# Kernel tuning notes

Hardware: AMD Instinct MI355X
Metric: run time of the kernel (lower is better)

Reference implementation:

```python
import jax, jax.numpy as jnp
import numpy as np
import math

B, S, D, H = 4, 2048, 1024, 16
DK = D // H

def setup_inputs() -> dict:
    key = jax.random.key(0)
    ks = jax.random.split(key, 8)
    scale = 1.0 / math.sqrt(D)
    q = jax.random.normal(ks[0], (B, S, D), dtype=jnp.float32)
    k = jax.random.normal(ks[1], (B, S, D), dtype=jnp.float32)
    v = jax.random.normal(ks[2], (B, S, D), dtype=jnp.float32)
    Wq = jax.random.normal(ks[3], (D, D), dtype=jnp.float32) * scale
    Wk = jax.random.normal(ks[4], (D, D), dtype=jnp.float32) * scale
    Wv = jax.random.normal(ks[5], (D, D), dtype=jnp.float32) * scale
    Wo = jax.random.normal(ks[6], (D, D), dtype=jnp.float32) * scale
    # causal mask, broadcast over batch and heads (masked_fill where mask == 0)
    mask = jnp.tril(jnp.ones((S, S), dtype=jnp.int32))[None, None, :, :]
    return {"q": q, "k": k, "v": v, "Wq": Wq, "Wk": Wk, "Wv": Wv, "Wo": Wo, "mask": mask}

def reference(q, k, v, Wq, Wk, Wv, Wo, mask):
    # Linear projections (nn.Linear: x @ W^T), split heads -> [B, H, S, DK]
    def split_heads(x, W):
        y = jnp.einsum('bsd,ed->bse', x, W)
        return y.reshape(x.shape[0], x.shape[1], H, DK).transpose(0, 2, 1, 3)
    qh = split_heads(q, Wq)
    kh = split_heads(k, Wk)
    vh = split_heads(v, Wv)
    scores = jnp.einsum('bhqd,bhkd->bhqk', qh, kh) / math.sqrt(DK)  # [B,H,S,S]
    scores = jnp.where(mask == 0, -jnp.inf, scores)
    p = jax.nn.softmax(scores, axis=-1)
    ctx = jnp.einsum('bhqk,bhkd->bhqd', p, vh)
    ctx = ctx.transpose(0, 2, 1, 3).reshape(q.shape[0], q.shape[1], H * DK)
    return jnp.einsum('bsd,ed->bse', ctx, Wo)
```

## Files before the change

kernel.cpp:

```cpp
#include <hip/hip_runtime.h>

#define BB 4
#define SS 2048
#define DD 1024
#define HH 16
#define DKK 64
#define MTOT (BB * SS)
#define QKV_N (MTOT * DD)
#define W_N (DD * DD)

typedef __attribute__((ext_vector_type(8))) short short8;
typedef __attribute__((ext_vector_type(4))) float f32x4;
typedef __attribute__((ext_vector_type(4))) unsigned short u16x4;
typedef unsigned short ushort_t;

#define GP(p) ((__attribute__((address_space(1))) void*)(p))
#define LP(p) ((__attribute__((address_space(3))) void*)(p))

#if __has_builtin(__builtin_amdgcn_exp2f)
#define EXP2(x) __builtin_amdgcn_exp2f(x)
#else
#define EXP2(x) __expf((x) * 0.6931471805599453f)
#endif
#define QSCALE 0.1803368801111204f

__device__ __forceinline__ ushort_t f2bf(float f) {
    union { float f; unsigned u; } c; c.f = f;
    unsigned r = c.u + 0x7fffu + ((c.u >> 16) & 1u);
    return (ushort_t)(r >> 16);
}

__global__ __launch_bounds__(256)
void cvt2(const float* __restrict__ s0, ushort_t* __restrict__ d0, int n0,
          const float* __restrict__ s1, ushort_t* __restrict__ d1, int n1)
{
    int i = (blockIdx.x * 256 + threadIdx.x) * 4;
    const float* s; ushort_t* d; int off;
    if (i < n0) { s = s0; d = d0; off = i; }
    else        { s = s1; d = d1; off = i - n0; if (off >= n1) return; }
    f32x4 x = *(const f32x4*)(s + off);
    u16x4 h;
    h[0] = f2bf(x[0]); h[1] = f2bf(x[1]); h[2] = f2bf(x[2]); h[3] = f2bf(x[3]);
    *(u16x4*)(d + off) = h;
}

template<int MODE>
__global__ __launch_bounds__(256, 2)
void gemm_m97(const ushort_t* __restrict__ A, const ushort_t* __restrict__ W,
              void* __restrict__ out, float scale)
{
    __shared__ ushort_t As[128 * 32];
    __shared__ ushort_t Bs[128 * 32];

    const int tid  = threadIdx.x;
    const int lane = tid & 63;
    const int w    = tid >> 6;
    const int wm   = w >> 1, wn = w & 1;
    const int l15  = lane & 15, l4 = lane >> 4;
    const int m0   = blockIdx.x * 128;
    const int n0   = blockIdx.y * 128;

    f32x4 acc[4][4] = {};

    for (int kk = 0; kk < 1024; kk += 32) {
        #pragma unroll
        for (int i = 0; i < 2; ++i) {
            int c  = i * 256 + w * 64 + lane;
            int r  = c >> 2;
            int cb = (c & 3) ^ (r & 3);
            __builtin_amdgcn_global_load_lds(
                GP(A + (size_t)(m0 + r) * 1024 + kk + cb * 8), LP(As + c * 8), 16, 0, 0);
            __builtin_amdgcn_global_load_lds(
                GP(W + (size_t)(n0 + r) * 1024 + kk + cb * 8), LP(Bs + c * 8), 16, 0, 0);
        }
        __syncthreads();

        short8 af[4], bfr[4];
        #pragma unroll
        for (int mi = 0; mi < 4; ++mi) {
            int row = wm * 64 + mi * 16 + l15;
            af[mi] = *(const short8*)(As + (row * 4 + (l4 ^ (row & 3))) * 8);
        }
        #pragma unroll
        for (int ni = 0; ni < 4; ++ni) {
            int row = wn * 64 + ni * 16 + l15;
            bfr[ni] = *(const short8*)(Bs + (row * 4 + (l4 ^ (row & 3))) * 8);
        }
        #pragma unroll
        for (int mi = 0; mi < 4; ++mi)
            #pragma unroll
            for (int ni = 0; ni < 4; ++ni)
                acc[mi][ni] = __builtin_amdgcn_mfma_f32_16x16x32_bf16(
                    af[mi], bfr[ni], acc[mi][ni], 0, 0, 0);
        __syncthreads();
    }

    #pragma unroll
    for (int mi = 0; mi < 4; ++mi) {
        int rowb = m0 + wm * 64 + mi * 16 + l4 * 4;
        #pragma unroll
        for (int ni = 0; ni < 4; ++ni) {
            int n = n0 + wn * 64 + ni * 16 + l15;
            if constexpr (MODE == 0) {
                int h = n >> 6, dk = n & 63;
                #pragma unroll
                for (int r = 0; r < 4; ++r) {
                    int m = rowb + r, b = m >> 11, s = m & 2047;
                    ((ushort_t*)out)[(((size_t)(b * 16 + h) * 2048 + s) << 6) + dk] =
                        f2bf(acc[mi][ni][r] * scale);
                }
            } else if constexpr (MODE == 1) {
                int h = n >> 6, dk = n & 63;
                int b = rowb >> 11, s0v = rowb & 2047;
                u16x4 hh;
                #pragma unroll
                for (int r = 0; r < 4; ++r) hh[r] = f2bf(acc[mi][ni][r]);
                *(u16x4*)((ushort_t*)out + (((size_t)(b * 16 + h) << 6) + dk) * 2048 + s0v) = hh;
            } else {
                #pragma unroll
                for (int r = 0; r < 4; ++r)
                    ((float*)out)[(size_t)(rowb + r) * 1024 + n] = acc[mi][ni][r];
            }
        }
    }
}

__global__ __launch_bounds__(256, 2)
void attn_fwd5(const ushort_t* __restrict__ Qh, const ushort_t* __restrict__ Kh,
               const ushort_t* __restrict__ Vt, ushort_t* __restrict__ Ctx)
{
    __shared__ ushort_t Kl[2][64 * 64];
    __shared__ ushort_t Vl[2][64 * 64];
    __shared__ ushort_t Pl[4][32][72];

    const int tid  = threadIdx.x;
    const int lane = tid & 63;
    const int w    = tid >> 6;
    const int l15  = lane & 15, l4 = lane >> 4;
    const int idx  = blockIdx.x;
    const int qt   = 15 - (idx >> 6);
    const int bh   = idx & 63;
    const int b    = bh >> 4, h = bh & 15;
    const int q0   = qt * 128;
    const ushort_t* Qb = Qh + (size_t)bh * SS * DKK;
    const ushort_t* Kb = Kh + (size_t)bh * SS * DKK;
    const ushort_t* Vb = Vt + (size_t)bh * DKK * SS;

    short8 qf[2][2];
    #pragma unroll
    for (int qg = 0; qg < 2; ++qg)
        #pragma unroll
        for (int ks = 0; ks < 2; ++ks) {
            int row = q0 + w * 32 + qg * 16 + l15;
            qf[qg][ks] = *(const short8*)(Qb + (size_t)row * 64 + ks * 32 + l4 * 8);
        }

    f32x4 Ot[2][4] = {};
    float m_i[2], l_i[2];
    m_i[0] = m_i[1] = -__builtin_inff();
    l_i[0] = l_i[1] = 0.f;

    auto stage = [&](int k0, ushort_t* Kd, ushort_t* Vd) {
        #pragma unroll
        for (int i = 0; i < 2; ++i) {
            int c  = i * 256 + tid;
            int r  = c >> 3;
            int cb = (c & 7) ^ (r & 7);
            __builtin_amdgcn_global_load_lds(
                GP(Kb + (size_t)(k0 + r) * 64 + cb * 8), LP(Kd + c * 8), 16, 0, 0);
            __builtin_amdgcn_global_load_lds(
                GP(Vb + (size_t)r * 2048 + k0 + cb * 8), LP(Vd + c * 8), 16, 0, 0);
        }
    };

    const int nkt = 2 * qt + 2;
    const int wrow0 = q0 + w * 32;
    stage(0, Kl[0], Vl[0]);

    for (int kt = 0; kt < nkt; ++kt) {
        const int k0 = kt * 64;
        __syncthreads();
        const ushort_t* Kc = Kl[kt & 1];
        const ushort_t* Vc = Vl[kt & 1];
        if (kt + 1 < nkt)
            stage(k0 + 64, Kl[(kt + 1) & 1], Vl[(kt + 1) & 1]);

        f32x4 sc[2][4] = {};
        #pragma unroll
        for (int ni = 0; ni < 4; ++ni) {
            short8 kf0, kf1;
            {
                int r = ni * 16 + l15;
                kf0 = *(const short8*)(Kc + (r * 8 + ((0 + l4) ^ (r & 7))) * 8);
                kf1 = *(const short8*)(Kc + (r * 8 + ((4 + l4) ^ (r & 7))) * 8);
            }
            #pragma unroll
            for (int qg = 0; qg < 2; ++qg) {
                sc[qg][ni] = __builtin_amdgcn_mfma_f32_16x16x32_bf16(
                    kf0, qf[qg][0], sc[qg][ni], 0, 0, 0);
                sc[qg][ni] = __builtin_amdgcn_mfma_f32_16x16x32_bf16(
                    kf1, qf[qg][1], sc[qg][ni], 0, 0, 0);
            }
        }

        if (k0 + 63 > wrow0) {
            #pragma unroll
            for (int qg = 0; qg < 2; ++qg) {
                int qrow = wrow0 + qg * 16 + l15;
                #pragma unroll
                for (int ni = 0; ni < 4; ++ni)
                    #pragma unroll
                    for (int r = 0; r < 4; ++r) {
                        int kcol = k0 + ni * 16 + l4 * 4 + r;
                        if (kcol > qrow) sc[qg][ni][r] = -1.0e30f;
                    }
            }
        }

        #pragma unroll
        for (int qg = 0; qg < 2; ++qg) {
            float mx = sc[qg][0][0];
            #pragma unroll
            for (int ni = 0; ni < 4; ++ni)
                #pragma unroll
                for (int r = 0; r < 4; ++r) mx = fmaxf(mx, sc[qg][ni][r]);
            mx = fmaxf(mx, __shfl_xor(mx, 16, 64));
            mx = fmaxf(mx, __shfl_xor(mx, 32, 64));
            float mnew  = fmaxf(m_i[qg], mx);
            float alpha = EXP2(m_i[qg] - mnew);
            float rs = 0.f;
            #pragma unroll
            for (int ni = 0; ni < 4; ++ni)
                #pragma unroll
                for (int r = 0; r < 4; ++r) {
                    float p = EXP2(sc[qg][ni][r] - mnew);
                    sc[qg][ni][r] = p;
                    rs += p;
                }
            rs += __shfl_xor(rs, 16, 64);
            rs += __shfl_xor(rs, 32, 64);
            l_i[qg] = l_i[qg] * alpha + rs;
            m_i[qg] = mnew;
            #pragma unroll
            for (int nd = 0; nd < 4; ++nd)
                #pragma unroll
                for (int r = 0; r < 4; ++r) Ot[qg][nd][r] *= alpha;
        }

        #pragma unroll
        for (int qg = 0; qg < 2; ++qg) {
            int qr = qg * 16 + l15;
            #pragma unroll
            for (int ni = 0; ni < 4; ++ni) {
                u16x4 hh;
                #pragma unroll
                for (int r = 0; r < 4; ++r) hh[r] = f2bf(sc[qg][ni][r]);
                *(u16x4*)(&Pl[w][qr][ni * 16 + l4 * 4]) = hh;
            }
        }

        short8 pT[2][2];
        #pragma unroll
        for (int qg = 0; qg < 2; ++qg)
            #pragma unroll
            for (int ks = 0; ks < 2; ++ks)
                pT[qg][ks] = *(const short8*)(&Pl[w][qg * 16 + l15][ks * 32 + l4 * 8]);

        #pragma unroll
        for (int nd = 0; nd < 4; ++nd) {
            short8 vf0, vf1;
            {
                int r = nd * 16 + l15;
                vf0 = *(const short8*)(Vc + (r * 8 + ((0 + l4) ^ (r & 7))) * 8);
                vf1 = *(const short8*)(Vc + (r * 8 + ((4 + l4) ^ (r & 7))) * 8);
            }
            #pragma unroll
            for (int qg = 0; qg < 2; ++qg) {
                Ot[qg][nd] = __builtin_amdgcn_mfma_f32_16x16x32_bf16(
                    vf0, pT[qg][0], Ot[qg][nd], 0, 0, 0);
                Ot[qg][nd] = __builtin_amdgcn_mfma_f32_16x16x32_bf16(
                    vf1, pT[qg][1], Ot[qg][nd], 0, 0, 0);
            }
        }
    }

    #pragma unroll
    for (int qg = 0; qg < 2; ++qg) {
        float inv = 1.0f / l_i[qg];
        int qrow = q0 + w * 32 + qg * 16 + l15;
        ushort_t* dst = Ctx + ((size_t)b * 2048 + qrow) * 1024 + h * 64;
        #pragma unroll
        for (int nd = 0; nd < 4; ++nd) {
            u16x4 hh;
            #pragma unroll
            for (int r = 0; r < 4; ++r) hh[r] = f2bf(Ot[qg][nd][r] * inv);
            *(u16x4*)(dst + nd * 16 + l4 * 4) = hh;
        }
    }
}

extern "C" void kernel_launch(void* const* d_in, const int* in_sizes, int n_in,
                              void* d_out, int out_size, void* d_ws, size_t ws_size,
                              hipStream_t stream)
{
    const float* q  = (const float*)d_in[0];
    const float* k  = (const float*)d_in[1];
    const float* v  = (const float*)d_in[2];
    const float* Wq = (const float*)d_in[3];
    const float* Wk = (const float*)d_in[4];
    const float* Wv = (const float*)d_in[5];
    const float* Wo = (const float*)d_in[6];
    float* out = (float*)d_out;

    ushort_t* B0 = (ushort_t*)d_ws;
    ushort_t* B1 = B0 + (size_t)QKV_N;
    ushort_t* B2 = B1 + (size_t)QKV_N;
    ushort_t* B3 = B2 + (size_t)QKV_N;
    ushort_t* wbE = (ushort_t*)d_out;
    dim3 gg(MTOT / 128, DD / 128);
    const int cvtg = (QKV_N + W_N) / 1024;

    cvt2<<<cvtg, 256, 0, stream>>>(q, B0, QKV_N, Wq, wbE, W_N);
    gemm_m97<0><<<gg, 256, 0, stream>>>(B0, wbE, B1, QSCALE);

    cvt2<<<cvtg, 256, 0, stream>>>(k, B0, QKV_N, Wk, wbE, W_N);
    gemm_m97<0><<<gg, 256, 0, stream>>>(B0, wbE, B2, 1.0f);

    cvt2<<<cvtg, 256, 0, stream>>>(v, B0, QKV_N, Wv, wbE, W_N);
    gemm_m97<1><<<gg, 256, 0, stream>>>(B0, wbE, B3, 1.0f);

    attn_fwd5<<<1024, 256, 0, stream>>>(B1, B2, B3, B0);

    cvt2<<<W_N / 1024, 256, 0, stream>>>(Wo, B1, W_N, Wo, B1, 0);
    gemm_m97<2><<<gg, 256, 0, stream>>>(B0, B1, out, 1.0f);
}
```

Before: 334.8 us.

## Double-buffer LDS tiles in projection GEMM to overlap loads with MFMA

```diff
diff --git a/kernel.cpp b/kernel.cpp
--- a/kernel.cpp
+++ b/kernel.cpp
@@ -45,12 +45,12 @@
 }
 
 template<int MODE>
-__global__ __launch_bounds__(256, 2)
-void gemm_m97(const ushort_t* __restrict__ A, const ushort_t* __restrict__ W,
-              void* __restrict__ out, float scale)
+__global__ __launch_bounds__(256, 3)
+void gemm_db(const ushort_t* __restrict__ A, const ushort_t* __restrict__ W,
+             void* __restrict__ out, float scale)
 {
-    __shared__ ushort_t As[128 * 32];
-    __shared__ ushort_t Bs[128 * 32];
+    __shared__ ushort_t As[2][128 * 32];
+    __shared__ ushort_t Bs[2][128 * 32];
 
     const int tid  = threadIdx.x;
     const int lane = tid & 63;
@@ -62,37 +62,42 @@
 
     f32x4 acc[4][4] = {};
 
-    for (int kk = 0; kk < 1024; kk += 32) {
+    auto stage = [&](int kk, int buf) {
         #pragma unroll
         for (int i = 0; i < 2; ++i) {
-            int c  = i * 256 + w * 64 + lane;
+            int c  = i * 256 + tid;
             int r  = c >> 2;
             int cb = (c & 3) ^ (r & 3);
             __builtin_amdgcn_global_load_lds(
-                GP(A + (size_t)(m0 + r) * 1024 + kk + cb * 8), LP(As + c * 8), 16, 0, 0);
+                GP(A + (size_t)(m0 + r) * 1024 + kk + cb * 8), LP(&As[buf][c * 8]), 16, 0, 0);
             __builtin_amdgcn_global_load_lds(
-                GP(W + (size_t)(n0 + r) * 1024 + kk + cb * 8), LP(Bs + c * 8), 16, 0, 0);
-        }
+                GP(W + (size_t)(n0 + r) * 1024 + kk + cb * 8), LP(&Bs[buf][c * 8]), 16, 0, 0);
+        }
+    };
+
+    stage(0, 0);
+
+    for (int it = 0; it < 32; ++it) {
         __syncthreads();
-
-        short8 af[4], bfr[4];
+        const ushort_t* Ac = As[it & 1];
+        const ushort_t* Bc = Bs[it & 1];
+        if (it + 1 < 32) stage((it + 1) * 32, (it + 1) & 1);
+
+        short8 bfr[4];
+        #pragma unroll
+        for (int ni = 0; ni < 4; ++ni) {
+            int row = wn * 64 + ni * 16 + l15;
+            bfr[ni] = *(const short8*)(Bc + (row * 4 + (l4 ^ (row & 3))) * 8);
+        }
         #pragma unroll
         for (int mi = 0; mi < 4; ++mi) {
             int row = wm * 64 + mi * 16 + l15;
-            af[mi] = *(const short8*)(As + (row * 4 + (l4 ^ (row & 3))) * 8);
-        }
-        #pragma unroll
-        for (int ni = 0; ni < 4; ++ni) {
-            int row = wn * 64 + ni * 16 + l15;
-            bfr[ni] = *(const short8*)(Bs + (row * 4 + (l4 ^ (row & 3))) * 8);
-        }
-        #pragma unroll
-        for (int mi = 0; mi < 4; ++mi)
+            short8 af = *(const short8*)(Ac + (row * 4 + (l4 ^ (row & 3))) * 8);
             #pragma unroll
             for (int ni = 0; ni < 4; ++ni)
                 acc[mi][ni] = __builtin_amdgcn_mfma_f32_16x16x32_bf16(
-                    af[mi], bfr[ni], acc[mi][ni], 0, 0, 0);
-        __syncthreads();
+                    af, bfr[ni], acc[mi][ni], 0, 0, 0);
+        }
     }
 
     #pragma unroll
@@ -321,16 +326,16 @@
     const int cvtg = (QKV_N + W_N) / 1024;
 
     cvt2<<<cvtg, 256, 0, stream>>>(q, B0, QKV_N, Wq, wbE, W_N);
-    gemm_m97<0><<<gg, 256, 0, stream>>>(B0, wbE, B1, QSCALE);
+    gemm_db<0><<<gg, 256, 0, stream>>>(B0, wbE, B1, QSCALE);
 
     cvt2<<<cvtg, 256, 0, stream>>>(k, B0, QKV_N, Wk, wbE, W_N);
-    gemm_m97<0><<<gg, 256, 0, stream>>>(B0, wbE, B2, 1.0f);
+    gemm_db<0><<<gg, 256, 0, stream>>>(B0, wbE, B2, 1.0f);
 
     cvt2<<<cvtg, 256, 0, stream>>>(v, B0, QKV_N, Wv, wbE, W_N);
-    gemm_m97<1><<<gg, 256, 0, stream>>>(B0, wbE, B3, 1.0f);
+    gemm_db<1><<<gg, 256, 0, stream>>>(B0, wbE, B3, 1.0f);
 
     attn_fwd5<<<1024, 256, 0, stream>>>(B1, B2, B3, B0);
 
     cvt2<<<W_N / 1024, 256, 0, stream>>>(Wo, B1, W_N, Wo, B1, 0);
-    gemm_m97<2><<<gg, 256, 0, stream>>>(B0, B1, out, 1.0f);
-}
+    gemm_db<2><<<gg, 256, 0, stream>>>(B0, B1, out, 1.0f);
+}
```

New measurement: 340.4 us. No clear change (+1.7%).
